# Kernel tuning notes

Measured on AMD Instinct MI355X. Metric: run time of the kernel, lower is better.

Reference implementation:

```python
import jax, jax.numpy as jnp
import numpy as np
import math

L = 2048
FANIN = 7
C = 64
N = 500000
NEG_SLOPE = 0.2


def setup_inputs() -> dict:
    key = jax.random.key(0)
    k1, k2, k3 = jax.random.split(key, 3)
    pos_ori = jax.random.normal(k1, (N, FANIN), dtype=jnp.float32)
    seq_idx = jax.random.randint(k2, (N,), 0, L, dtype=jnp.int32)
    # kaiming_uniform_1 bound per source: sqrt(6/(1+k^2) * fanin) with fanin = l*7*C
    fanin = L * FANIN * C
    bound = math.sqrt(6.0 / (1.0 + NEG_SLOPE ** 2) * fanin)
    W = jax.random.uniform(k3, (L, FANIN, C), dtype=jnp.float32,
                           minval=-bound, maxval=bound)
    # scale down to avoid overflow in fp32 demo while keeping same math form
    W = W * 1e-3
    b = jnp.zeros((L, C), dtype=jnp.float32)
    return {"pos_ori": pos_ori, "seq_idx": seq_idx, "W": W, "b": b}


def reference(pos_ori, seq_idx, W, b):
    # gather per-sample weight [N,7,C] and bias [N,C]
    Wg = W[seq_idx]              # [N, 7, C]
    bg = b[seq_idx]              # [N, C]
    # 1x7 . 7xC batched matmul, fused with bias add and LeakyReLU
    y = jnp.einsum('nk,nkc->nc', pos_ori, Wg) + bg  # [N, C]
    return jnp.where(y >= 0, y, NEG_SLOPE * y)
```

## Files before the change

### kernel.cpp

```cpp
#include <hip/hip_runtime.h>


typedef float f32x4 __attribute__((ext_vector_type(4)));

#define FANIN 7
#define C 64
#define NEG_SLOPE 0.2f

__global__ __launch_bounds__(256) void weightnet_kernel(
    const float* __restrict__ pos,
    const int*   __restrict__ seq,
    const float* __restrict__ W,
    const float* __restrict__ B,
    float*       __restrict__ out,
    int n_total)
{
    long gid = (long)blockIdx.x * 256 + threadIdx.x;
    if (gid >= (long)n_total * 16) return;
    int n  = (int)(gid >> 4);
    int c  = ((int)gid & 15) << 2;

    int idx = seq[n];

    const float* pn = pos + (size_t)n * FANIN;
    float p[FANIN];
    #pragma unroll
    for (int k = 0; k < FANIN; ++k) p[k] = pn[k];

    const f32x4* Wp = (const f32x4*)(W + (size_t)idx * (FANIN * C) + c);
    f32x4 acc = *(const f32x4*)(B + (size_t)idx * C + c);
    #pragma unroll
    for (int k = 0; k < FANIN; ++k) {
        f32x4 w = Wp[(size_t)k * (C / 4)];
        acc += p[k] * w;
    }

    acc.x = acc.x >= 0.f ? acc.x : NEG_SLOPE * acc.x;
    acc.y = acc.y >= 0.f ? acc.y : NEG_SLOPE * acc.y;
    acc.z = acc.z >= 0.f ? acc.z : NEG_SLOPE * acc.z;
    acc.w = acc.w >= 0.f ? acc.w : NEG_SLOPE * acc.w;

    __builtin_nontemporal_store(acc, (f32x4*)(out + (size_t)n * C + c));
}

extern "C" void kernel_launch(void* const* d_in, const int* in_sizes, int n_in,
                              void* d_out, int out_size, void* d_ws, size_t ws_size,
                              hipStream_t stream) {
    const float* pos = (const float*)d_in[0];
    const int*   seq = (const int*)d_in[1];
    const float* W   = (const float*)d_in[2];
    const float* B   = (const float*)d_in[3];
    float* out = (float*)d_out;

    int n_total = in_sizes[1];
    long total_threads = (long)n_total * 16;
    int blocks = (int)((total_threads + 255) / 256);
    weightnet_kernel<<<blocks, 256, 0, stream>>>(pos, seq, W, B, out, n_total);
}
```

Baseline: 192.4 us.

## Cooperatively load pos/seq per wave and broadcast via shuffles, 8 channels per thread

Each wave now handles 8 samples. It loads their pos rows and seq indices with coalesced per-lane loads and hands them to the other lanes through cross-lane shuffles, replacing the redundant scalar loads each thread made before. Each thread now computes two float4 channel groups instead of one, halving the thread count and doubling the work per thread. This cuts duplicate global load traffic and instruction count, in exchange for shuffle overhead and fewer threads to hide memory latency.

```diff
diff --git a/kernel.cpp b/kernel.cpp
--- a/kernel.cpp
+++ b/kernel.cpp
@@ -7,6 +7,14 @@
 #define C 64
 #define NEG_SLOPE 0.2f
 
+__device__ __forceinline__ f32x4 lrelu4(f32x4 a) {
+    a.x = a.x >= 0.f ? a.x : NEG_SLOPE * a.x;
+    a.y = a.y >= 0.f ? a.y : NEG_SLOPE * a.y;
+    a.z = a.z >= 0.f ? a.z : NEG_SLOPE * a.z;
+    a.w = a.w >= 0.f ? a.w : NEG_SLOPE * a.w;
+    return a;
+}
+
 __global__ __launch_bounds__(256) void weightnet_kernel(
     const float* __restrict__ pos,
     const int*   __restrict__ seq,
@@ -15,32 +23,48 @@
     float*       __restrict__ out,
     int n_total)
 {
-    long gid = (long)blockIdx.x * 256 + threadIdx.x;
-    if (gid >= (long)n_total * 16) return;
-    int n  = (int)(gid >> 4);
-    int c  = ((int)gid & 15) << 2;
+    int tid  = threadIdx.x;
+    int lane = tid & 63;
+    int grp  = lane >> 3;
+    int sub  = lane & 7;
 
-    int idx = seq[n];
+    long wave_id = (long)blockIdx.x * 4 + (tid >> 6);
+    long n_base  = wave_id * 8;
+    int  n       = (int)(n_base + grp);
 
-    const float* pn = pos + (size_t)n * FANIN;
+    float pv = 0.f;
+    long pofs = n_base * FANIN + lane;
+    if (lane < 56 && pofs < (long)n_total * FANIN) pv = pos[pofs];
+    int sv = 0;
+    if (lane < 8 && n_base + lane < n_total) sv = seq[n_base + lane];
+
+    int idx = __shfl(sv, grp, 64);
     float p[FANIN];
     #pragma unroll
-    for (int k = 0; k < FANIN; ++k) p[k] = pn[k];
+    for (int k = 0; k < FANIN; ++k) p[k] = __shfl(pv, grp * FANIN + k, 64);
 
-    const f32x4* Wp = (const f32x4*)(W + (size_t)idx * (FANIN * C) + c);
-    f32x4 acc = *(const f32x4*)(B + (size_t)idx * C + c);
+    if (n >= n_total) return;
+
+    int c = sub << 2;
+    const float* Wn = W + (size_t)idx * (FANIN * C);
+    const float* Bn = B + (size_t)idx * C;
+
+    f32x4 acc0 = *(const f32x4*)(Bn + c);
+    f32x4 acc1 = *(const f32x4*)(Bn + c + 32);
     #pragma unroll
     for (int k = 0; k < FANIN; ++k) {
-        f32x4 w = Wp[(size_t)k * (C / 4)];
-        acc += p[k] * w;
+        f32x4 w0 = *(const f32x4*)(Wn + k * C + c);
+        f32x4 w1 = *(const f32x4*)(Wn + k * C + c + 32);
+        acc0 += p[k] * w0;
+        acc1 += p[k] * w1;
     }
 
-    acc.x = acc.x >= 0.f ? acc.x : NEG_SLOPE * acc.x;
-    acc.y = acc.y >= 0.f ? acc.y : NEG_SLOPE * acc.y;
-    acc.z = acc.z >= 0.f ? acc.z : NEG_SLOPE * acc.z;
-    acc.w = acc.w >= 0.f ? acc.w : NEG_SLOPE * acc.w;
+    acc0 = lrelu4(acc0);
+    acc1 = lrelu4(acc1);
 
-    __builtin_nontemporal_store(acc, (f32x4*)(out + (size_t)n * C + c));
+    float* on = out + (size_t)n * C;
+    __builtin_nontemporal_store(acc0, (f32x4*)(on + c));
+    __builtin_nontemporal_store(acc1, (f32x4*)(on + c + 32));
 }
 
 extern "C" void kernel_launch(void* const* d_in, const int* in_sizes, int n_in,
@@ -53,7 +77,6 @@
     float* out = (float*)d_out;
 
     int n_total = in_sizes[1];
-    long total_threads = (long)n_total * 16;
-    int blocks = (int)((total_threads + 255) / 256);
+    int blocks = (n_total + 31) / 32;
     weightnet_kernel<<<blocks, 256, 0, stream>>>(pos, seq, W, B, out, n_total);
 }
```

Result: faster. 187.1 us (-2.7%).
